# Optimization experiments

Measured on AMD Instinct MI355X. Metric: run time of the kernel, lower is better.

The kernel has to match this reference:

```python
import jax, jax.numpy as jnp
import numpy as np

D_MODEL = 1024
NHEAD = 16
D_K = D_MODEL // NHEAD
BATCH = 8
SEQ = 1024
SPARSITY = 0.9


def setup_inputs() -> dict:
    key = jax.random.key(0)
    ks = jax.random.split(key, 13)
    q = jax.random.normal(ks[0], (BATCH, SEQ, D_MODEL), dtype=jnp.float32)
    k = jax.random.normal(ks[1], (BATCH, SEQ, D_MODEL), dtype=jnp.float32)
    v = jax.random.normal(ks[2], (BATCH, SEQ, D_MODEL), dtype=jnp.float32)
    mask = jax.random.uniform(ks[3], (BATCH, NHEAD, SEQ, SEQ)) > SPARSITY
    s = 1.0 / np.sqrt(D_MODEL)  # nn.Linear-style init scale
    def lin(kw, kb):
        W = jax.random.uniform(kw, (D_MODEL, D_MODEL), minval=-s, maxval=s, dtype=jnp.float32)
        b = jax.random.uniform(kb, (D_MODEL,), minval=-s, maxval=s, dtype=jnp.float32)
        return W, b
    Wq, bq = lin(ks[4], ks[5])
    Wk, bk = lin(ks[6], ks[7])
    Wv, bv = lin(ks[8], ks[9])
    Wo, bo = lin(ks[10], ks[11])
    return {"query": q, "key": k, "value": v, "mask": mask,
            "Wq": Wq, "bq": bq, "Wk": Wk, "bk": bk,
            "Wv": Wv, "bv": bv, "Wo": Wo, "bo": bo}


def reference(query, key, value, mask, Wq, bq, Wk, bk, Wv, bv, Wo, bo):
    B, S, _ = query.shape
    # projections (torch Linear: x @ W.T + b), split into heads -> [B, H, S, d_k]
    def proj(x, W, b):
        return (x @ W.T + b).reshape(B, S, NHEAD, D_K).transpose(0, 2, 1, 3)
    Q = proj(query, Wq, bq)
    K = proj(key, Wk, bk)
    V = proj(value, Wv, bv)
    scale = 1.0 / jnp.sqrt(jnp.float32(D_K))
    scores = jnp.einsum('bhqd,bhkd->bhqk', Q, K) * scale  # [B,H,S,S]
    scores = jnp.where(mask, scores, -jnp.inf)
    attn = jax.nn.softmax(scores, axis=-1)
    out = jnp.einsum('bhqk,bhkd->bhqd', attn, V)           # [B,H,S,d_k]
    out = out.transpose(0, 2, 1, 3).reshape(B, S, D_MODEL)
    return out @ Wo.T + bo
```

## Files before the change

kernel.cpp:

```cpp
#include <hip/hip_runtime.h>

typedef __bf16 bf16;
typedef bf16 bf16x4 __attribute__((ext_vector_type(4)));
typedef bf16 bf16x8 __attribute__((ext_vector_type(8)));
typedef float f32x4 __attribute__((ext_vector_type(4)));

#define D_MODEL 1024
#define NHEAD   16
#define D_K     64
#define BATCH   8
#define SEQL    1024
#define MROWS   (BATCH*SEQL)

struct Cvt7 {
    const float* s[7];
    bf16*        d[7];
    int          n[7];
};

__global__ __launch_bounds__(256) void cvt7_kernel(Cvt7 a) {
    const int y = blockIdx.y;
    const float* __restrict__ src = a.s[y];
    bf16* __restrict__ dst = a.d[y];
    const int n4 = a.n[y] >> 2;
    const int stride = gridDim.x * blockDim.x;
    for (int i = blockIdx.x * blockDim.x + threadIdx.x; i < n4; i += stride) {
        float4 v = ((const float4*)src)[i];
        bf16x4 o = { (bf16)v.x, (bf16)v.y, (bf16)v.z, (bf16)v.w };
        ((bf16x4*)dst)[i] = o;
    }
}

#define BM 128
#define BN 128
#define BK 32

__device__ __forceinline__ void gemm_core(const bf16* __restrict__ A, const bf16* __restrict__ B,
                                          int bm, int bn, int K,
                                          bf16* lA, bf16* lB, f32x4 (&acc)[4][4]) {
    const int t = threadIdx.x;
    const int lane = t & 63, w = t >> 6;
    const int wr = w >> 1, wc = w & 1;
    const int r = lane & 15, kb = lane >> 4;

    for (int k0 = 0; k0 < K; k0 += BK) {
        __syncthreads();
        #pragma unroll
        for (int i = 0; i < 2; ++i) {
            const int off = i * 4096 + w * 1024 + lane * 16;
            const int row = off >> 6;
            const int cb  = off & 63;
            const bf16* srcA = A + (size_t)(bm + row) * K + k0 + (cb >> 1);
            const bf16* srcB = B + (size_t)(bn + row) * K + k0 + (cb >> 1);
            __builtin_amdgcn_global_load_lds(
                (const __attribute__((address_space(1))) unsigned int*)srcA,
                (__attribute__((address_space(3))) unsigned int*)((char*)lA + i * 4096 + w * 1024),
                16, 0, 0);
            __builtin_amdgcn_global_load_lds(
                (const __attribute__((address_space(1))) unsigned int*)srcB,
                (__attribute__((address_space(3))) unsigned int*)((char*)lB + i * 4096 + w * 1024),
                16, 0, 0);
        }
        __syncthreads();

        bf16x8 af[4], bfr[4];
        #pragma unroll
        for (int m = 0; m < 4; ++m)
            af[m] = *(const bf16x8*)(lA + (wr * 64 + m * 16 + r) * BK + kb * 8);
        #pragma unroll
        for (int n = 0; n < 4; ++n)
            bfr[n] = *(const bf16x8*)(lB + (wc * 64 + n * 16 + r) * BK + kb * 8);
        #pragma unroll
        for (int m = 0; m < 4; ++m)
            #pragma unroll
            for (int n = 0; n < 4; ++n)
                acc[m][n] = __builtin_amdgcn_mfma_f32_16x16x32_bf16(af[m], bfr[n], acc[m][n], 0, 0, 0);
    }
}

__global__ __launch_bounds__(256) void proj3_kernel(
        const bf16* __restrict__ xq, const bf16* __restrict__ xk, const bf16* __restrict__ xv,
        const bf16* __restrict__ Wqb, const bf16* __restrict__ Wkb, const bf16* __restrict__ Wvb,
        const float* __restrict__ bq, const float* __restrict__ bk, const float* __restrict__ bv,
        bf16* __restrict__ Qp, bf16* __restrict__ Kp, bf16* __restrict__ Vt) {
    __shared__ bf16 lA[BM * BK], lB[BN * BK];
    const int z = blockIdx.z;
    const bf16* A    = (z == 0) ? xq  : (z == 1) ? xk  : xv;
    const bf16* Bm   = (z == 0) ? Wqb : (z == 1) ? Wkb : Wvb;
    const float* bias = (z == 0) ? bq : (z == 1) ? bk  : bv;
    const int bm = blockIdx.x * BM, bn = blockIdx.y * BN;

    f32x4 acc[4][4] = {};
    gemm_core(A, Bm, bm, bn, D_MODEL, lA, lB, acc);

    const int lane = threadIdx.x & 63, w = threadIdx.x >> 6;
    const int wr = w >> 1, wc = w & 1, r = lane & 15, g = lane >> 4;
    #pragma unroll
    for (int n = 0; n < 4; ++n) {
        const int col = bn + wc * 64 + n * 16 + r;
        const float bvl = bias[col];
        const int h = col >> 6, d = col & 63;
        #pragma unroll
        for (int m = 0; m < 4; ++m) {
            #pragma unroll
            for (int j = 0; j < 4; ++j) {
                const int row = bm + wr * 64 + m * 16 + g * 4 + j;
                const float v = acc[m][n][j] + bvl;
                const int b = row >> 10, s = row & (SEQL - 1);
                const int bh = b * NHEAD + h;
                if (z == 0) {
                    Qp[((size_t)bh * SEQL + s) * D_K + d] = (bf16)v;
                } else if (z == 1) {
                    Kp[((size_t)bh * SEQL + s) * D_K + d] = (bf16)v;
                } else {
                    Vt[((size_t)bh * D_K + d) * SEQL + s] = (bf16)v;
                }
            }
        }
    }
}

__global__ __launch_bounds__(256) void outproj_kernel(
        const bf16* __restrict__ AO, const bf16* __restrict__ Wob,
        const float* __restrict__ bo, float* __restrict__ out) {
    __shared__ bf16 lA[BM * BK], lB[BN * BK];
    const int bm = blockIdx.x * BM, bn = blockIdx.y * BN;
    f32x4 acc[4][4] = {};
    gemm_core(AO, Wob, bm, bn, D_MODEL, lA, lB, acc);

    const int lane = threadIdx.x & 63, w = threadIdx.x >> 6;
    const int wr = w >> 1, wc = w & 1, r = lane & 15, g = lane >> 4;
    #pragma unroll
    for (int n = 0; n < 4; ++n) {
        const int col = bn + wc * 64 + n * 16 + r;
        const float bvl = bo[col];
        #pragma unroll
        for (int m = 0; m < 4; ++m)
            #pragma unroll
            for (int j = 0; j < 4; ++j) {
                const int row = bm + wr * 64 + m * 16 + g * 4 + j;
                out[(size_t)row * D_MODEL + col] = acc[m][n][j] + bvl;
            }
    }
}

__global__ __launch_bounds__(256, 4) void attn_kernel(
        const bf16* __restrict__ Qp, const bf16* __restrict__ Kp, const bf16* __restrict__ Vt,
        const unsigned int* __restrict__ mask, bf16* __restrict__ AO) {
    __shared__ char kbuf[8192];
    __shared__ char vbuf[8192];
    __shared__ char mbuf[16384];
    const int lin = blockIdx.x + blockIdx.y * gridDim.x;
    const int xcd = lin & 7, pos = lin >> 3;
    const int bh  = xcd * 16 + (pos >> 4);
    const int qt  = pos & 15;
    const int b = bh >> 4, h = bh & 15;
    const int t = threadIdx.x, lane = t & 63, w = t >> 6;
    const int q0 = qt * 64;
    const int r = lane & 15, g = lane >> 4;

    const char* __restrict__ Kb = (const char*)(Kp + (size_t)bh * SEQL * D_K);
    const char* __restrict__ Vb = (const char*)(Vt + (size_t)bh * D_K * SEQL);
    const char* __restrict__ Mb = (const char*)(mask + ((size_t)bh * SEQL + q0) * SEQL);

    const bf16* __restrict__ Qh = Qp + ((size_t)bh * SEQL + q0 + w * 16) * D_K;
    bf16x8 qf[2];
    #pragma unroll
    for (int kk = 0; kk < 2; ++kk)
        qf[kk] = *(const bf16x8*)(Qh + r * D_K + kk * 32 + g * 8);

    f32x4 o[4] = {};
    float psum = 0.f;
    char* P = mbuf + w * 4096;
    const int swz = (r & 7) << 4;

    for (int s0 = 0; s0 < SEQL; s0 += 64) {
        __syncthreads();
        #pragma unroll
        for (int i = 0; i < 2; ++i) {
            const int slot = i * 256 + t;
            const int row = slot >> 3, ch = slot & 7;
            const char* srcK = Kb + (size_t)(s0 + row) * 128 + ((ch * 16) ^ ((row & 7) << 4));
            const char* srcV = Vb + (size_t)row * (SEQL * 2) + s0 * 2 + ((ch * 16) ^ ((row & 7) << 4));
            __builtin_amdgcn_global_load_lds(
                (const __attribute__((address_space(1))) unsigned int*)srcK,
                (__attribute__((address_space(3))) unsigned int*)(kbuf + i * 4096 + w * 1024),
                16, 0, 0);
            __builtin_amdgcn_global_load_lds(
                (const __attribute__((address_space(1))) unsigned int*)srcV,
                (__attribute__((address_space(3))) unsigned int*)(vbuf + i * 4096 + w * 1024),
                16, 0, 0);
        }
        #pragma unroll
        for (int i = 0; i < 4; ++i) {
            const int slot = i * 256 + t;
            const int row = slot >> 4, ch = slot & 15;
            const char* srcM = Mb + (size_t)row * (SEQL * 4) + s0 * 4 + ((ch * 16) ^ ((row & 7) << 4));
            __builtin_amdgcn_global_load_lds(
                (const __attribute__((address_space(1))) unsigned int*)srcM,
                (__attribute__((address_space(3))) unsigned int*)(mbuf + i * 4096 + w * 1024),
                16, 0, 0);
        }
        __syncthreads();

        f32x4 sf[4] = {};
        __builtin_amdgcn_s_setprio(1);
        #pragma unroll
        for (int n = 0; n < 4; ++n) {
            #pragma unroll
            for (int kk = 0; kk < 2; ++kk) {
                const int krow = n * 16 + r;
                bf16x8 kf = *(const bf16x8*)(kbuf + krow * 128 + ((kk * 64 + g * 16) ^ swz));
                sf[n] = __builtin_amdgcn_mfma_f32_16x16x32_bf16(kf, qf[kk], sf[n], 0, 0, 0);
            }
        }
        __builtin_amdgcn_s_setprio(0);
        const int mrow = w * 16 + r;
        uint4 mv[4];
        #pragma unroll
        for (int n = 0; n < 4; ++n)
            mv[n] = *(const uint4*)(mbuf + mrow * 256 + ((n * 64 + g * 16) ^ swz));
        #pragma unroll
        for (int n = 0; n < 4; ++n) {
            const float p0 = mv[n].x ? __expf(sf[n][0] * 0.125f) : 0.f;
            const float p1 = mv[n].y ? __expf(sf[n][1] * 0.125f) : 0.f;
            const float p2 = mv[n].z ? __expf(sf[n][2] * 0.125f) : 0.f;
            const float p3 = mv[n].w ? __expf(sf[n][3] * 0.125f) : 0.f;
            psum += (p0 + p1) + (p2 + p3);
            bf16x4 pb = { (bf16)p0, (bf16)p1, (bf16)p2, (bf16)p3 };
            *(bf16x4*)(P + ((r * 128 + n * 32 + g * 8) ^ swz)) = pb;
        }
        bf16x8 pf0 = *(const bf16x8*)(P + ((r * 128 + 0 * 64 + g * 16) ^ swz));
        bf16x8 pf1 = *(const bf16x8*)(P + ((r * 128 + 1 * 64 + g * 16) ^ swz));
        __builtin_amdgcn_s_setprio(1);
        #pragma unroll
        for (int n = 0; n < 4; ++n) {
            const int vrow = n * 16 + r;
            bf16x8 vf0 = *(const bf16x8*)(vbuf + vrow * 128 + ((0 * 64 + g * 16) ^ swz));
            bf16x8 vf1 = *(const bf16x8*)(vbuf + vrow * 128 + ((1 * 64 + g * 16) ^ swz));
            o[n] = __builtin_amdgcn_mfma_f32_16x16x32_bf16(vf0, pf0, o[n], 0, 0, 0);
            o[n] = __builtin_amdgcn_mfma_f32_16x16x32_bf16(vf1, pf1, o[n], 0, 0, 0);
        }
        __builtin_amdgcn_s_setprio(0);
    }

    psum += __shfl_xor(psum, 16);
    psum += __shfl_xor(psum, 32);
    const float inv = 1.0f / psum;

    const size_t rowbase = ((size_t)(b * SEQL + q0 + w * 16 + r)) * D_MODEL + h * D_K;
    #pragma unroll
    for (int n = 0; n < 4; ++n) {
        bf16x4 ob = { (bf16)(o[n][0] * inv), (bf16)(o[n][1] * inv),
                      (bf16)(o[n][2] * inv), (bf16)(o[n][3] * inv) };
        *(bf16x4*)(AO + rowbase + n * 16 + g * 4) = ob;
    }
}

extern "C" void kernel_launch(void* const* d_in, const int* in_sizes, int n_in,
                              void* d_out, int out_size, void* d_ws, size_t ws_size,
                              hipStream_t stream) {
    const float* q    = (const float*)d_in[0];
    const float* k    = (const float*)d_in[1];
    const float* v    = (const float*)d_in[2];
    const unsigned int* mask = (const unsigned int*)d_in[3];
    const float* Wq = (const float*)d_in[4];
    const float* bq = (const float*)d_in[5];
    const float* Wk = (const float*)d_in[6];
    const float* bk = (const float*)d_in[7];
    const float* Wv = (const float*)d_in[8];
    const float* bv = (const float*)d_in[9];
    const float* Wo = (const float*)d_in[10];
    const float* bo = (const float*)d_in[11];

    char* ws = (char*)d_ws;
    const size_t MB = 1u << 20;
    bf16* qb  = (bf16*)(ws + 0 * MB);
    bf16* kb  = (bf16*)(ws + 16 * MB);
    bf16* vb  = (bf16*)(ws + 32 * MB);
    bf16* Wqb = (bf16*)(ws + 48 * MB);
    bf16* Wkb = (bf16*)(ws + 50 * MB);
    bf16* Wvb = (bf16*)(ws + 52 * MB);
    bf16* Wob = (bf16*)(ws + 54 * MB);
    bf16* Qp  = (bf16*)(ws + 56 * MB);
    bf16* Kp  = (bf16*)(ws + 72 * MB);
    bf16* Vt  = (bf16*)(ws + 88 * MB);
    bf16* AO  = (bf16*)(ws + 104 * MB);

    Cvt7 c;
    c.s[0] = q;  c.d[0] = qb;  c.n[0] = MROWS * D_MODEL;
    c.s[1] = k;  c.d[1] = kb;  c.n[1] = MROWS * D_MODEL;
    c.s[2] = v;  c.d[2] = vb;  c.n[2] = MROWS * D_MODEL;
    c.s[3] = Wq; c.d[3] = Wqb; c.n[3] = D_MODEL * D_MODEL;
    c.s[4] = Wk; c.d[4] = Wkb; c.n[4] = D_MODEL * D_MODEL;
    c.s[5] = Wv; c.d[5] = Wvb; c.n[5] = D_MODEL * D_MODEL;
    c.s[6] = Wo; c.d[6] = Wob; c.n[6] = D_MODEL * D_MODEL;
    cvt7_kernel<<<dim3(1024, 7), 256, 0, stream>>>(c);

    proj3_kernel<<<dim3(MROWS / BM, D_MODEL / BN, 3), 256, 0, stream>>>(
        qb, kb, vb, Wqb, Wkb, Wvb, bq, bk, bv, Qp, Kp, Vt);

    attn_kernel<<<dim3(SEQL / 64, BATCH * NHEAD), 256, 0, stream>>>(Qp, Kp, Vt, mask, AO);

    outproj_kernel<<<dim3(MROWS / BM, D_MODEL / BN), 256, 0, stream>>>(AO, Wob, bo, (float*)d_out);
}
```

Before: 293.1 us.

## Process 128 query rows per attention block to reuse K/V tiles

Doubles the attention kernel's query tile from 64 to 128 rows, with each wave handling two 16-row sub-tiles. Each K/V tile staged into LDS now serves twice as many queries, and K fragments are hoisted into registers and reused across both sub-tiles. This halves K/V global traffic and LDS staging per query. The mask buffer doubles to 32 KB and register pressure rises, so occupancy drops (launch bound lowered to 3) and the grid halves.

```diff
diff --git a/kernel.cpp b/kernel.cpp
--- a/kernel.cpp
+++ b/kernel.cpp
@@ -144,34 +144,36 @@
     }
 }
 
-__global__ __launch_bounds__(256, 4) void attn_kernel(
+__global__ __launch_bounds__(256, 3) void attn_kernel(
         const bf16* __restrict__ Qp, const bf16* __restrict__ Kp, const bf16* __restrict__ Vt,
         const unsigned int* __restrict__ mask, bf16* __restrict__ AO) {
     __shared__ char kbuf[8192];
     __shared__ char vbuf[8192];
-    __shared__ char mbuf[16384];
+    __shared__ char mbuf[32768];
     const int lin = blockIdx.x + blockIdx.y * gridDim.x;
     const int xcd = lin & 7, pos = lin >> 3;
-    const int bh  = xcd * 16 + (pos >> 4);
-    const int qt  = pos & 15;
+    const int bh  = xcd * 16 + (pos >> 3);
+    const int qt  = pos & 7;
     const int b = bh >> 4, h = bh & 15;
     const int t = threadIdx.x, lane = t & 63, w = t >> 6;
-    const int q0 = qt * 64;
+    const int q0 = qt * 128;
     const int r = lane & 15, g = lane >> 4;
 
     const char* __restrict__ Kb = (const char*)(Kp + (size_t)bh * SEQL * D_K);
     const char* __restrict__ Vb = (const char*)(Vt + (size_t)bh * D_K * SEQL);
     const char* __restrict__ Mb = (const char*)(mask + ((size_t)bh * SEQL + q0) * SEQL);
 
-    const bf16* __restrict__ Qh = Qp + ((size_t)bh * SEQL + q0 + w * 16) * D_K;
-    bf16x8 qf[2];
+    const bf16* __restrict__ Qh = Qp + ((size_t)bh * SEQL + q0 + w * 32) * D_K;
+    bf16x8 qf[2][2];
     #pragma unroll
-    for (int kk = 0; kk < 2; ++kk)
-        qf[kk] = *(const bf16x8*)(Qh + r * D_K + kk * 32 + g * 8);
-
-    f32x4 o[4] = {};
-    float psum = 0.f;
-    char* P = mbuf + w * 4096;
+    for (int qq = 0; qq < 2; ++qq)
+        #pragma unroll
+        for (int kk = 0; kk < 2; ++kk)
+            qf[qq][kk] = *(const bf16x8*)(Qh + (qq * 16 + r) * D_K + kk * 32 + g * 8);
+
+    f32x4 o[2][4] = {};
+    float psum[2] = {0.f, 0.f};
+    char* P = mbuf + w * 8192;
     const int swz = (r & 7) << 4;
 
     for (int s0 = 0; s0 < SEQL; s0 += 64) {
@@ -192,7 +194,7 @@
                 16, 0, 0);
         }
         #pragma unroll
-        for (int i = 0; i < 4; ++i) {
+        for (int i = 0; i < 8; ++i) {
             const int slot = i * 256 + t;
             const int row = slot >> 4, ch = slot & 15;
             const char* srcM = Mb + (size_t)row * (SEQL * 4) + s0 * 4 + ((ch * 16) ^ ((row & 7) << 4));
@@ -203,57 +205,74 @@
         }
         __syncthreads();
 
-        f32x4 sf[4] = {};
+        bf16x8 kf[4][2];
+        #pragma unroll
+        for (int n = 0; n < 4; ++n)
+            #pragma unroll
+            for (int kk = 0; kk < 2; ++kk)
+                kf[n][kk] = *(const bf16x8*)(kbuf + (n * 16 + r) * 128 + ((kk * 64 + g * 16) ^ swz));
+        f32x4 sf[2][4] = {};
         __builtin_amdgcn_s_setprio(1);
         #pragma unroll
-        for (int n = 0; n < 4; ++n) {
-            #pragma unroll
-            for (int kk = 0; kk < 2; ++kk) {
-                const int krow = n * 16 + r;
-                bf16x8 kf = *(const bf16x8*)(kbuf + krow * 128 + ((kk * 64 + g * 16) ^ swz));
-                sf[n] = __builtin_amdgcn_mfma_f32_16x16x32_bf16(kf, qf[kk], sf[n], 0, 0, 0);
+        for (int qq = 0; qq < 2; ++qq)
+            #pragma unroll
+            for (int n = 0; n < 4; ++n)
+                #pragma unroll
+                for (int kk = 0; kk < 2; ++kk)
+                    sf[qq][n] = __builtin_amdgcn_mfma_f32_16x16x32_bf16(kf[n][kk], qf[qq][kk], sf[qq][n], 0, 0, 0);
+        __builtin_amdgcn_s_setprio(0);
+        #pragma unroll
+        for (int qq = 0; qq < 2; ++qq) {
+            const int mrow = w * 32 + qq * 16 + r;
+            uint4 mv[4];
+            #pragma unroll
+            for (int n = 0; n < 4; ++n)
+                mv[n] = *(const uint4*)(mbuf + mrow * 256 + ((n * 64 + g * 16) ^ swz));
+            #pragma unroll
+            for (int n = 0; n < 4; ++n) {
+                const float p0 = mv[n].x ? __expf(sf[qq][n][0] * 0.125f) : 0.f;
+                const float p1 = mv[n].y ? __expf(sf[qq][n][1] * 0.125f) : 0.f;
+                const float p2 = mv[n].z ? __expf(sf[qq][n][2] * 0.125f) : 0.f;
+                const float p3 = mv[n].w ? __expf(sf[qq][n][3] * 0.125f) : 0.f;
+                psum[qq] += (p0 + p1) + (p2 + p3);
+                bf16x4 pb = { (bf16)p0, (bf16)p1, (bf16)p2, (bf16)p3 };
+                *(bf16x4*)(P + (((qq * 16 + r) * 128 + n * 32 + g * 8) ^ swz)) = pb;
             }
         }
-        __builtin_amdgcn_s_setprio(0);
-        const int mrow = w * 16 + r;
-        uint4 mv[4];
-        #pragma unroll
-        for (int n = 0; n < 4; ++n)
-            mv[n] = *(const uint4*)(mbuf + mrow * 256 + ((n * 64 + g * 16) ^ swz));
-        #pragma unroll
-        for (int n = 0; n < 4; ++n) {
-            const float p0 = mv[n].x ? __expf(sf[n][0] * 0.125f) : 0.f;
-            const float p1 = mv[n].y ? __expf(sf[n][1] * 0.125f) : 0.f;
-            const float p2 = mv[n].z ? __expf(sf[n][2] * 0.125f) : 0.f;
-            const float p3 = mv[n].w ? __expf(sf[n][3] * 0.125f) : 0.f;
-            psum += (p0 + p1) + (p2 + p3);
-            bf16x4 pb = { (bf16)p0, (bf16)p1, (bf16)p2, (bf16)p3 };
-            *(bf16x4*)(P + ((r * 128 + n * 32 + g * 8) ^ swz)) = pb;
-        }
-        bf16x8 pf0 = *(const bf16x8*)(P + ((r * 128 + 0 * 64 + g * 16) ^ swz));
-        bf16x8 pf1 = *(const bf16x8*)(P + ((r * 128 + 1 * 64 + g * 16) ^ swz));
+        bf16x8 pf[2][2];
+        #pragma unroll
+        for (int qq = 0; qq < 2; ++qq)
+            #pragma unroll
+            for (int kk = 0; kk < 2; ++kk)
+                pf[qq][kk] = *(const bf16x8*)(P + (((qq * 16 + r) * 128 + kk * 64 + g * 16) ^ swz));
         __builtin_amdgcn_s_setprio(1);
         #pragma unroll
         for (int n = 0; n < 4; ++n) {
             const int vrow = n * 16 + r;
             bf16x8 vf0 = *(const bf16x8*)(vbuf + vrow * 128 + ((0 * 64 + g * 16) ^ swz));
             bf16x8 vf1 = *(const bf16x8*)(vbuf + vrow * 128 + ((1 * 64 + g * 16) ^ swz));
-            o[n] = __builtin_amdgcn_mfma_f32_16x16x32_bf16(vf0, pf0, o[n], 0, 0, 0);
-            o[n] = __builtin_amdgcn_mfma_f32_16x16x32_bf16(vf1, pf1, o[n], 0, 0, 0);
+            #pragma unroll
+            for (int qq = 0; qq < 2; ++qq) {
+                o[qq][n] = __builtin_amdgcn_mfma_f32_16x16x32_bf16(vf0, pf[qq][0], o[qq][n], 0, 0, 0);
+                o[qq][n] = __builtin_amdgcn_mfma_f32_16x16x32_bf16(vf1, pf[qq][1], o[qq][n], 0, 0, 0);
+            }
         }
         __builtin_amdgcn_s_setprio(0);
     }
 
-    psum += __shfl_xor(psum, 16);
-    psum += __shfl_xor(psum, 32);
-    const float inv = 1.0f / psum;
-
-    const size_t rowbase = ((size_t)(b * SEQL + q0 + w * 16 + r)) * D_MODEL + h * D_K;
     #pragma unroll
-    for (int n = 0; n < 4; ++n) {
-        bf16x4 ob = { (bf16)(o[n][0] * inv), (bf16)(o[n][1] * inv),
-                      (bf16)(o[n][2] * inv), (bf16)(o[n][3] * inv) };
-        *(bf16x4*)(AO + rowbase + n * 16 + g * 4) = ob;
+    for (int qq = 0; qq < 2; ++qq) {
+        float ps = psum[qq];
+        ps += __shfl_xor(ps, 16);
+        ps += __shfl_xor(ps, 32);
+        const float inv = 1.0f / ps;
+        const size_t rowbase = ((size_t)(b * SEQL + q0 + w * 32 + qq * 16 + r)) * D_MODEL + h * D_K;
+        #pragma unroll
+        for (int n = 0; n < 4; ++n) {
+            bf16x4 ob = { (bf16)(o[qq][n][0] * inv), (bf16)(o[qq][n][1] * inv),
+                          (bf16)(o[qq][n][2] * inv), (bf16)(o[qq][n][3] * inv) };
+            *(bf16x4*)(AO + rowbase + n * 16 + g * 4) = ob;
+        }
     }
 }
 
@@ -300,7 +319,7 @@
     proj3_kernel<<<dim3(MROWS / BM, D_MODEL / BN, 3), 256, 0, stream>>>(
         qb, kb, vb, Wqb, Wkb, Wvb, bq, bk, bv, Qp, Kp, Vt);
 
-    attn_kernel<<<dim3(SEQL / 64, BATCH * NHEAD), 256, 0, stream>>>(Qp, Kp, Vt, mask, AO);
+    attn_kernel<<<dim3(SEQL / 128, BATCH * NHEAD), 256, 0, stream>>>(Qp, Kp, Vt, mask, AO);
 
     outproj_kernel<<<dim3(MROWS / BM, D_MODEL / BN), 256, 0, stream>>>(AO, Wob, bo, (float*)d_out);
 }
```

Result: slower. 300.3 us (+2.5%).
